# Performance work log

Measured on AMD Instinct MI355X. Metric: run time of the kernel, lower is better.

Reference implementation:

```python
import jax, jax.numpy as jnp
import numpy as np

F, G, S, E, P, B, T = 1024, 512, 512, 256, 8, 256, 256

def _gru(x, h, W_ih, W_hh, b_ih, b_hh):
    # torch.nn.GRUCell math; gate order r, z, n
    gi = x @ W_ih.T + b_ih
    gh = h @ W_hh.T + b_hh
    ir, iz, inn = jnp.split(gi, 3, axis=1)
    hr, hz, hn = jnp.split(gh, 3, axis=1)
    r = jax.nn.sigmoid(ir + hr)
    z = jax.nn.sigmoid(iz + hz)
    n = jnp.tanh(inn + r * hn)
    return (1.0 - z) * n + z * h

def setup_inputs() -> dict:
    key = jax.random.key(0)
    ks = jax.random.split(key, 16)
    feature_ = jax.random.normal(ks[0], (B, F), dtype=jnp.float32)
    spk_id = jax.random.randint(ks[1], (B,), 0, P)
    speaker_mask = jax.nn.one_hot(spk_id, P, dtype=jnp.float32)
    global_history = jax.random.normal(ks[2], (T, B, G), dtype=jnp.float32)
    speaker0 = jax.random.normal(ks[3], (B, P, S), dtype=jnp.float32)
    emotion0 = jax.random.normal(ks[4], (B, E), dtype=jnp.float32)
    sc = 0.05
    return {
        "feature_": feature_, "speaker_mask": speaker_mask,
        "global_history": global_history, "speaker0": speaker0, "emotion0": emotion0,
        "Wg_ih": jax.random.normal(ks[5], (3 * G, F + S)) * sc,
        "Wg_hh": jax.random.normal(ks[6], (3 * G, G)) * sc,
        "bg_ih": jnp.zeros((3 * G,)), "bg_hh": jnp.zeros((3 * G,)),
        "Wp_ih": jax.random.normal(ks[7], (3 * S, F + G)) * sc,
        "Wp_hh": jax.random.normal(ks[8], (3 * S, S)) * sc,
        "bp_ih": jnp.zeros((3 * S,)), "bp_hh": jnp.zeros((3 * S,)),
        "We_ih": jax.random.normal(ks[9], (3 * E, S)) * sc,
        "We_hh": jax.random.normal(ks[10], (3 * E, E)) * sc,
        "be_ih": jnp.zeros((3 * E,)), "be_hh": jnp.zeros((3 * E,)),
        "attn_W": jax.random.normal(ks[11], (G, F)) * sc,
    }

def reference(feature_, speaker_mask, global_history, speaker0, emotion0,
              Wg_ih, Wg_hh, bg_ih, bg_hh,
              Wp_ih, Wp_hh, bp_ih, bp_hh,
              We_ih, We_hh, be_ih, be_hh, attn_W):
    b = feature_.shape[0]
    p = speaker_mask.shape[1]
    spk_id = jnp.argmax(speaker_mask, axis=1)                      # (B,)
    rows = jnp.arange(b)
    sel0 = speaker0[rows, spk_id]                                   # select_parties -> (B, S)
    feature_speak = jnp.concatenate([feature_, sel0], axis=1)       # (B, F+S)
    global_state = _gru(feature_speak, global_history[-1], Wg_ih, Wg_hh, bg_ih, bg_hh)
    # attention over global history (T > 0 path); dropout = identity (eval)
    x_ = feature_ @ attn_W.T                                        # (B, G)
    alpha = jax.nn.softmax(jnp.einsum('bg,tbg->bt', x_, global_history), axis=1)
    context = jnp.einsum('bt,tbg->bg', alpha, global_history)       # (B, G)
    feature_context = jnp.concatenate([feature_, context], axis=1)  # (B, F+G)
    fc = jnp.broadcast_to(feature_context[:, None, :], (b, p, feature_context.shape[1]))
    fc = fc.reshape(b * p, -1)
    parties_state = _gru(fc, speaker0.reshape(b * p, -1), Wp_ih, Wp_hh, bp_ih, bp_hh)
    parties_state = parties_state.reshape(b, p, -1)                 # (B, P, S)
    m = speaker_mask[:, :, None]
    speaker = speaker0 * (1.0 - m) + parties_state * m
    parties = speaker[rows, spk_id]                                 # (B, S)
    emotion = _gru(parties, emotion0, We_ih, We_hh, be_ih, be_hh)
    return emotion, global_state, speaker
```

## Files before the change

### kernel.cpp

```cpp
#include <hip/hip_runtime.h>
#include <hip/hip_bf16.h>
#include <math.h>

#define BB 256
#define FF 1024
#define GG 512
#define SS 512
#define EE 256
#define PP 8
#define TT 256

typedef __attribute__((ext_vector_type(8))) short bs8;
typedef __attribute__((ext_vector_type(4))) float f32x4;

__device__ __forceinline__ float sigmoidf_(float x) { return 1.0f / (1.0f + expf(-x)); }

__device__ __forceinline__ short f2bf(float f) {
    union { float f; unsigned u; } v; v.f = f;
    unsigned r = v.u + 0x7FFFu + ((v.u >> 16) & 1u);
    return (short)(r >> 16);
}

union BPack { bs8 s; __hip_bfloat162 h[4]; };

__device__ __forceinline__ bs8 ld8cvt(const float* p) {
    float4 a = *(const float4*)p, b = *(const float4*)(p + 4);
    BPack u;
    u.h[0] = __float22bfloat162_rn({a.x, a.y});
    u.h[1] = __float22bfloat162_rn({a.z, a.w});
    u.h[2] = __float22bfloat162_rn({b.x, b.y});
    u.h[3] = __float22bfloat162_rn({b.z, b.w});
    return u.s;
}
__device__ __forceinline__ void ld8split(const float* p, bs8& ho, bs8& lo) {
    float4 a = *(const float4*)p, b = *(const float4*)(p + 4);
    float v[8] = {a.x, a.y, a.z, a.w, b.x, b.y, b.z, b.w};
    BPack uh, ul;
#pragma unroll
    for (int j = 0; j < 4; ++j) {
        __hip_bfloat162 h2 = __float22bfloat162_rn({v[2*j], v[2*j+1]});
        uh.h[j] = h2;
        float r0 = v[2*j]   - __low2float(h2);
        float r1 = v[2*j+1] - __high2float(h2);
        ul.h[j] = __float22bfloat162_rn({r0, r1});
    }
    ho = uh.s; lo = ul.s;
}

#define OWG_IH 0L
#define OWG_HH 2359296L
#define OWP_IH 3145728L
#define OWP_HH 5505024L
#define OWE_IH 6291456L
#define OWE_HH 6684672L
#define WTOT   6881280L

#define MB1 3360
#define MB2 3616
#define MB3 3744
#define MB4 3808
#define MB5 3840
#define MB6 4096
#define MBE 5120

__global__ __launch_bounds__(256) void k_mega(
        const float* __restrict__ Wg_ih, const float* __restrict__ Wg_hh,
        const float* __restrict__ Wp_ih, const float* __restrict__ Wp_hh,
        const float* __restrict__ We_ih, const float* __restrict__ We_hh,
        const float* __restrict__ attn_W, const float* __restrict__ feature_,
        const float* __restrict__ h_g, const float* __restrict__ emotion0,
        const float* __restrict__ mask, const float* __restrict__ sp0,
        short* __restrict__ Wbf, short* __restrict__ awhi, short* __restrict__ awlo,
        short* __restrict__ xg, short* __restrict__ fhi, short* __restrict__ flo,
        short* __restrict__ hg_bf, short* __restrict__ emo_bf, short* __restrict__ sel0_bf,
        float* __restrict__ sel0, int* __restrict__ spk, float* __restrict__ speaker_out) {
    int blk = blockIdx.x, tid = threadIdx.x;
    if (blk < MB1) {
        long i = (long)blk * 2048 + tid * 8;
        const float* src; long base;
        if      (i < OWG_HH) { src = Wg_ih; base = OWG_IH; }
        else if (i < OWP_IH) { src = Wg_hh; base = OWG_HH; }
        else if (i < OWP_HH) { src = Wp_ih; base = OWP_IH; }
        else if (i < OWE_IH) { src = Wp_hh; base = OWP_HH; }
        else if (i < OWE_HH) { src = We_ih; base = OWE_IH; }
        else                 { src = We_hh; base = OWE_HH; }
        *(bs8*)(Wbf + i) = ld8cvt(src + (i - base));
    } else if (blk < MB2) {
        long i = (long)(blk - MB1) * 2048 + tid * 8;
        bs8 h, l;
        ld8split(attn_W + i, h, l);
        *(bs8*)(awhi + i) = h;
        *(bs8*)(awlo + i) = l;
    } else if (blk < MB3) {
        long i = (long)(blk - MB2) * 2048 + tid * 8;
        bs8 h, l;
        ld8split(feature_ + i, h, l);
        *(bs8*)(fhi + i) = h;
        *(bs8*)(flo + i) = l;
        long b = i >> 10, c = i & 1023;
        *(bs8*)(xg + b * 1536 + c) = h;
    } else if (blk < MB4) {
        long i = (long)(blk - MB3) * 2048 + tid * 8;
        *(bs8*)(hg_bf + i) = ld8cvt(h_g + i);
    } else if (blk < MB5) {
        long i = (long)(blk - MB4) * 2048 + tid * 8;
        *(bs8*)(emo_bf + i) = ld8cvt(emotion0 + i);
    } else if (blk < MB6) {
        int b = blk - MB5;
        __shared__ int sid;
        if (tid == 0) {
            int best = 0; float bv = mask[b * PP];
            for (int p = 1; p < PP; ++p) { float v = mask[b * PP + p]; if (v > bv) { bv = v; best = p; } }
            sid = best; spk[b] = best;
        }
        __syncthreads();
        const float* src = sp0 + ((size_t)b * PP + sid) * SS;
        for (int j = tid; j < SS; j += 256) {
            float v = src[j];
            sel0[(size_t)b * SS + j] = v;
            short h = f2bf(v);
            sel0_bf[(size_t)b * SS + j] = h;
            xg[(size_t)b * 1536 + FF + j] = h;
        }
    } else {
        size_t i = ((size_t)(blk - MB6) * 256 + tid) * 4;
        *(float4*)(speaker_out + i) = *(const float4*)(sp0 + i);
    }
}

struct GDesc {
    const short *A, *A2, *W, *Wl;
    float* C;
    int lda, lda2, kb, ldw, woff, ldc, K, nbn, flags;
};
struct GBatch {
    GDesc d[6];
    int start[7];
    int ng;
};

__global__ __launch_bounds__(256) void k_bgemm(GBatch gb) {
    __shared__ __align__(16) short Ash[64 * 64], Bsh[64 * 64];
    __shared__ __align__(16) short Asl[64 * 64], Bsl[64 * 64];

    int bid = blockIdx.x;
    int g = 0;
    while (g + 1 < gb.ng && bid >= gb.start[g + 1]) ++g;
    GDesc d = gb.d[g];
    int local = bid - gb.start[g];
    int bn = local % d.nbn, bm = local / d.nbn;
    const bool split = (d.flags & 1) != 0;

    const int tid = threadIdx.x;
    const int lane = tid & 63, wid = tid >> 6;
    const int wr = wid >> 1, wc = wid & 1;
    const int r0 = tid >> 3, c0 = tid & 7;
    const int r1 = r0 + 32;
    const int la = lane & 15, lk = lane >> 4;
    const int sw = la & 7;

    f32x4 acc[2][2] = {};

    for (int k0 = 0; k0 < d.K; k0 += 64) {
        bs8 ah0, ah1, bh0, bh1, al0, al1, bl0, bl1;
        if (split) {
            size_t oa0 = (size_t)(bm * 64 + r0) * d.lda + k0 + c0 * 8;
            size_t oa1 = (size_t)(bm * 64 + r1) * d.lda + k0 + c0 * 8;
            size_t ow0 = (size_t)(bn * 64 + r0) * d.ldw + d.woff + k0 + c0 * 8;
            size_t ow1 = (size_t)(bn * 64 + r1) * d.ldw + d.woff + k0 + c0 * 8;
            ah0 = *(const bs8*)(d.A + oa0);  ah1 = *(const bs8*)(d.A + oa1);
            al0 = *(const bs8*)(d.A2 + oa0); al1 = *(const bs8*)(d.A2 + oa1);
            bh0 = *(const bs8*)(d.W + ow0);  bh1 = *(const bs8*)(d.W + ow1);
            bl0 = *(const bs8*)(d.Wl + ow0); bl1 = *(const bs8*)(d.Wl + ow1);
        } else {
            const short* Ab; int alda;
            if (k0 < d.kb) { Ab = d.A + k0; alda = d.lda; }
            else           { Ab = d.A2 + (k0 - d.kb); alda = d.lda2; }
            ah0 = *(const bs8*)(Ab + (size_t)(bm * 64 + r0) * alda + c0 * 8);
            ah1 = *(const bs8*)(Ab + (size_t)(bm * 64 + r1) * alda + c0 * 8);
            bh0 = *(const bs8*)(d.W + (size_t)(bn * 64 + r0) * d.ldw + d.woff + k0 + c0 * 8);
            bh1 = *(const bs8*)(d.W + (size_t)(bn * 64 + r1) * d.ldw + d.woff + k0 + c0 * 8);
        }
        __syncthreads();
        *(bs8*)(Ash + r0 * 64 + ((c0 ^ (r0 & 7)) * 8)) = ah0;
        *(bs8*)(Ash + r1 * 64 + ((c0 ^ (r1 & 7)) * 8)) = ah1;
        *(bs8*)(Bsh + r0 * 64 + ((c0 ^ (r0 & 7)) * 8)) = bh0;
        *(bs8*)(Bsh + r1 * 64 + ((c0 ^ (r1 & 7)) * 8)) = bh1;
        if (split) {
            *(bs8*)(Asl + r0 * 64 + ((c0 ^ (r0 & 7)) * 8)) = al0;
            *(bs8*)(Asl + r1 * 64 + ((c0 ^ (r1 & 7)) * 8)) = al1;
            *(bs8*)(Bsl + r0 * 64 + ((c0 ^ (r0 & 7)) * 8)) = bl0;
            *(bs8*)(Bsl + r1 * 64 + ((c0 ^ (r1 & 7)) * 8)) = bl1;
        }
        __syncthreads();
#pragma unroll
        for (int kk = 0; kk < 2; ++kk) {
            int slot = kk * 4 + lk;
            int off = (slot ^ sw) * 8;
            bs8 a0 = *(const bs8*)(Ash + (wr * 32 + la) * 64      + off);
            bs8 a1 = *(const bs8*)(Ash + (wr * 32 + 16 + la) * 64 + off);
            bs8 b0 = *(const bs8*)(Bsh + (wc * 32 + la) * 64      + off);
            bs8 b1 = *(const bs8*)(Bsh + (wc * 32 + 16 + la) * 64 + off);
            acc[0][0] = __builtin_amdgcn_mfma_f32_16x16x32_bf16(a0, b0, acc[0][0], 0, 0, 0);
            acc[0][1] = __builtin_amdgcn_mfma_f32_16x16x32_bf16(a0, b1, acc[0][1], 0, 0, 0);
            acc[1][0] = __builtin_amdgcn_mfma_f32_16x16x32_bf16(a1, b0, acc[1][0], 0, 0, 0);
            acc[1][1] = __builtin_amdgcn_mfma_f32_16x16x32_bf16(a1, b1, acc[1][1], 0, 0, 0);
            if (split) {
                bs8 xl0 = *(const bs8*)(Asl + (wr * 32 + la) * 64      + off);
                bs8 xl1 = *(const bs8*)(Asl + (wr * 32 + 16 + la) * 64 + off);
                bs8 yl0 = *(const bs8*)(Bsl + (wc * 32 + la) * 64      + off);
                bs8 yl1 = *(const bs8*)(Bsl + (wc * 32 + 16 + la) * 64 + off);
                acc[0][0] = __builtin_amdgcn_mfma_f32_16x16x32_bf16(a0, yl0, acc[0][0], 0, 0, 0);
                acc[0][0] = __builtin_amdgcn_mfma_f32_16x16x32_bf16(xl0, b0, acc[0][0], 0, 0, 0);
                acc[0][1] = __builtin_amdgcn_mfma_f32_16x16x32_bf16(a0, yl1, acc[0][1], 0, 0, 0);
                acc[0][1] = __builtin_amdgcn_mfma_f32_16x16x32_bf16(xl0, b1, acc[0][1], 0, 0, 0);
                acc[1][0] = __builtin_amdgcn_mfma_f32_16x16x32_bf16(a1, yl0, acc[1][0], 0, 0, 0);
                acc[1][0] = __builtin_amdgcn_mfma_f32_16x16x32_bf16(xl1, b0, acc[1][0], 0, 0, 0);
                acc[1][1] = __builtin_amdgcn_mfma_f32_16x16x32_bf16(a1, yl1, acc[1][1], 0, 0, 0);
                acc[1][1] = __builtin_amdgcn_mfma_f32_16x16x32_bf16(xl1, b1, acc[1][1], 0, 0, 0);
            }
        }
    }

    const int rowb = (lane >> 4) * 4, coln = lane & 15;
    const bool accum = (d.flags & 2) != 0;
#pragma unroll
    for (int i = 0; i < 2; ++i)
#pragma unroll
    for (int j = 0; j < 2; ++j)
#pragma unroll
    for (int r = 0; r < 4; ++r) {
        int row = bm * 64 + wr * 32 + i * 16 + rowb + r;
        int col = bn * 64 + wc * 32 + j * 16 + coln;
        size_t idx = (size_t)row * d.ldc + col;
        if (accum) d.C[idx] += acc[i][j][r];
        else       d.C[idx]  = acc[i][j][r];
    }
}

__global__ __launch_bounds__(256) void k_attnp(const float* __restrict__ x_,
                                               const float* __restrict__ gh,
                                               float* __restrict__ ctxp,
                                               float2* __restrict__ msb) {
    int blk = blockIdx.x;
    int b = blk & (BB - 1), ch = blk >> 8;
    int tid = threadIdx.x, w = tid >> 6, lane = tid & 63;
    __shared__ float wm[4], ws[4];
    __shared__ float part[4][GG];

    const float* xb = x_ + (size_t)b * GG + lane * 8;
    float4 xa = *(const float4*)xb;
    float4 xc = *(const float4*)(xb + 4);

    float m = -INFINITY, s = 0.f;
    float acc[8] = {};
    int t0 = ch * 32 + w * 8;
#pragma unroll
    for (int it = 0; it < 8; ++it) {
        int t = t0 + it;
        const float* row = gh + ((size_t)t * BB + b) * GG + lane * 8;
        float4 v1 = *(const float4*)row;
        float4 v2 = *(const float4*)(row + 4);
        float p = v1.x*xa.x + v1.y*xa.y + v1.z*xa.z + v1.w*xa.w
                + v2.x*xc.x + v2.y*xc.y + v2.z*xc.z + v2.w*xc.w;
#pragma unroll
        for (int off = 32; off; off >>= 1) p += __shfl_xor(p, off);
        float nm = fmaxf(m, p);
        float scale = expf(m - nm);
        float e = expf(p - nm);
        s = s * scale + e;
        acc[0] = acc[0]*scale + e*v1.x; acc[1] = acc[1]*scale + e*v1.y;
        acc[2] = acc[2]*scale + e*v1.z; acc[3] = acc[3]*scale + e*v1.w;
        acc[4] = acc[4]*scale + e*v2.x; acc[5] = acc[5]*scale + e*v2.y;
        acc[6] = acc[6]*scale + e*v2.z; acc[7] = acc[7]*scale + e*v2.w;
        m = nm;
    }
    if (lane == 0) { wm[w] = m; ws[w] = s; }
    *(float4*)&part[w][lane * 8]     = make_float4(acc[0], acc[1], acc[2], acc[3]);
    *(float4*)&part[w][lane * 8 + 4] = make_float4(acc[4], acc[5], acc[6], acc[7]);
    __syncthreads();

    float M = fmaxf(fmaxf(wm[0], wm[1]), fmaxf(wm[2], wm[3]));
    float f0 = expf(wm[0] - M), f1 = expf(wm[1] - M);
    float f2 = expf(wm[2] - M), f3 = expf(wm[3] - M);
    if (tid == 0) {
        float S = ws[0]*f0 + ws[1]*f1 + ws[2]*f2 + ws[3]*f3;
        msb[blk] = make_float2(M, S);
    }
    for (int j = tid; j < GG; j += 256) {
        float r = part[0][j]*f0 + part[1][j]*f1 + part[2][j]*f2 + part[3][j]*f3;
        ctxp[(size_t)blk * GG + j] = r;
    }
}

__global__ __launch_bounds__(256) void k_attnm(const float* __restrict__ ctxp,
                                               const float2* __restrict__ msb,
                                               short* __restrict__ ctx_bf) {
    int b = blockIdx.x, tid = threadIdx.x;
    float mv[8], sv[8];
    float M = -INFINITY;
#pragma unroll
    for (int c = 0; c < 8; ++c) {
        float2 t = msb[c * BB + b];
        mv[c] = t.x; sv[c] = t.y;
        M = fmaxf(M, t.x);
    }
    float S = 0.f;
    float f[8];
#pragma unroll
    for (int c = 0; c < 8; ++c) { f[c] = expf(mv[c] - M); S += sv[c] * f[c]; }
    float inv = 1.0f / S;
#pragma unroll
    for (int c = 0; c < 8; ++c) f[c] *= inv;
    for (int j = tid; j < GG; j += 256) {
        float r = 0.f;
#pragma unroll
        for (int c = 0; c < 8; ++c) r += ctxp[(size_t)(c * BB + b) * GG + j] * f[c];
        ctx_bf[(size_t)b * GG + j] = f2bf(r);
    }
}

__global__ __launch_bounds__(256) void k_gru2(
        const float* __restrict__ gi_g, const float* __restrict__ gh_g,
        const float* __restrict__ bg_ih, const float* __restrict__ bg_hh,
        const float* __restrict__ hg, float* __restrict__ global_out,
        const float* __restrict__ gi_p, const float* __restrict__ gh_p,
        const float* __restrict__ bp_ih, const float* __restrict__ bp_hh,
        const float* __restrict__ sel0, const int* __restrict__ spk,
        short* __restrict__ par_bf, float* __restrict__ speaker_out) {
    int idx = blockIdx.x * 256 + threadIdx.x;
    if (idx < BB * GG) {
        int b = idx / GG, j = idx - b * GG;
        const float* gib = gi_g + (size_t)b * 3 * GG;
        const float* ghb = gh_g + (size_t)b * 3 * GG;
        float r = sigmoidf_(gib[j] + bg_ih[j] + ghb[j] + bg_hh[j]);
        float z = sigmoidf_(gib[GG + j] + bg_ih[GG + j] + ghb[GG + j] + bg_hh[GG + j]);
        float n = tanhf(gib[2*GG + j] + bg_ih[2*GG + j] + r * (ghb[2*GG + j] + bg_hh[2*GG + j]));
        global_out[idx] = (1.0f - z) * n + z * hg[idx];
    } else {
        idx -= BB * GG;
        int b = idx / SS, j = idx - b * SS;
        const float* gib = gi_p + (size_t)b * 3 * SS;
        const float* ghb = gh_p + (size_t)b * 3 * SS;
        float r = sigmoidf_(gib[j] + bp_ih[j] + ghb[j] + bp_hh[j]);
        float z = sigmoidf_(gib[SS + j] + bp_ih[SS + j] + ghb[SS + j] + bp_hh[SS + j]);
        float n = tanhf(gib[2*SS + j] + bp_ih[2*SS + j] + r * (ghb[2*SS + j] + bp_hh[2*SS + j]));
        float o = (1.0f - z) * n + z * sel0[idx];
        par_bf[idx] = f2bf(o);
        speaker_out[((size_t)b * PP + spk[b]) * SS + j] = o;
    }
}

__global__ __launch_bounds__(256) void k_gru(const float* __restrict__ gi, const float* __restrict__ gh,
                                             const float* __restrict__ bih, const float* __restrict__ bhh,
                                             const float* __restrict__ h,
                                             float* __restrict__ out, int H) {
    int idx = blockIdx.x * 256 + threadIdx.x;
    int b = idx / H, j = idx - b * H;
    const float* gib = gi + (size_t)b * 3 * H;
    const float* ghb = gh + (size_t)b * 3 * H;
    float r = sigmoidf_(gib[j] + bih[j] + ghb[j] + bhh[j]);
    float z = sigmoidf_(gib[H + j] + bih[H + j] + ghb[H + j] + bhh[H + j]);
    float n = tanhf(gib[2 * H + j] + bih[2 * H + j] + r * (ghb[2 * H + j] + bhh[2 * H + j]));
    out[idx] = (1.0f - z) * n + z * h[idx];
}

extern "C" void kernel_launch(void* const* d_in, const int* in_sizes, int n_in,
                              void* d_out, int out_size, void* d_ws, size_t ws_size,
                              hipStream_t stream) {
    const float* feature_ = (const float*)d_in[0];
    const float* mask     = (const float*)d_in[1];
    const float* ghist    = (const float*)d_in[2];
    const float* speaker0 = (const float*)d_in[3];
    const float* emotion0 = (const float*)d_in[4];
    const float* Wg_ih    = (const float*)d_in[5];
    const float* Wg_hh    = (const float*)d_in[6];
    const float* bg_ih    = (const float*)d_in[7];
    const float* bg_hh    = (const float*)d_in[8];
    const float* Wp_ih    = (const float*)d_in[9];
    const float* Wp_hh    = (const float*)d_in[10];
    const float* bp_ih    = (const float*)d_in[11];
    const float* bp_hh    = (const float*)d_in[12];
    const float* We_ih    = (const float*)d_in[13];
    const float* We_hh    = (const float*)d_in[14];
    const float* be_ih    = (const float*)d_in[15];
    const float* be_hh    = (const float*)d_in[16];
    const float* attn_W   = (const float*)d_in[17];

    float* out = (float*)d_out;
    float* emotion_out = out;
    float* global_out  = out + (size_t)BB * EE;
    float* speaker_out = global_out + (size_t)BB * GG;

    char* cur = (char*)d_ws;
    short* Wbf     = (short*)cur; cur += (size_t)WTOT * 2;
    short* awhi    = (short*)cur; cur += (size_t)GG * FF * 2;
    short* awlo    = (short*)cur; cur += (size_t)GG * FF * 2;
    short* xg      = (short*)cur; cur += (size_t)BB * 1536 * 2;
    short* fhi     = (short*)cur; cur += (size_t)BB * FF * 2;
    short* flo     = (short*)cur; cur += (size_t)BB * FF * 2;
    short* hg_bf   = (short*)cur; cur += (size_t)BB * GG * 2;
    short* emo_bf  = (short*)cur; cur += (size_t)BB * EE * 2;
    short* sel0_bf = (short*)cur; cur += (size_t)BB * SS * 2;
    short* ctx_bf  = (short*)cur; cur += (size_t)BB * GG * 2;
    short* par_bf  = (short*)cur; cur += (size_t)BB * SS * 2;

    float* sel0    = (float*)cur; cur += (size_t)BB * SS * 4;
    float* x_      = (float*)cur; cur += (size_t)BB * GG * 4;
    float* ctxp    = (float*)cur; cur += (size_t)2048 * GG * 4;
    float2* msb    = (float2*)cur; cur += (size_t)2048 * 8;
    float* gi_g    = (float*)cur; cur += (size_t)BB * 3 * GG * 4;
    float* gh_g    = (float*)cur; cur += (size_t)BB * 3 * GG * 4;
    float* gi_p    = (float*)cur; cur += (size_t)BB * 3 * SS * 4;
    float* gh_p    = (float*)cur; cur += (size_t)BB * 3 * SS * 4;
    float* gi_e    = (float*)cur; cur += (size_t)BB * 3 * EE * 4;
    float* gh_e    = (float*)cur; cur += (size_t)BB * 3 * EE * 4;
    int*   spk     = (int*)cur;   cur += 256 * 4;

    const float* h_g = ghist + (size_t)(TT - 1) * BB * GG;

    short* Wg_ih_bf = Wbf + OWG_IH;
    short* Wg_hh_bf = Wbf + OWG_HH;
    short* Wp_ih_bf = Wbf + OWP_IH;
    short* Wp_hh_bf = Wbf + OWP_HH;
    short* We_ih_bf = Wbf + OWE_IH;
    short* We_hh_bf = Wbf + OWE_HH;

    k_mega<<<MBE, 256, 0, stream>>>(Wg_ih, Wg_hh, Wp_ih, Wp_hh, We_ih, We_hh,
                                    attn_W, feature_, h_g, emotion0, mask, speaker0,
                                    Wbf, awhi, awlo, xg, fhi, flo, hg_bf, emo_bf,
                                    sel0_bf, sel0, spk, speaker_out);

    GBatch gbA;
    gbA.d[0] = { fhi, flo, awhi, awlo, x_, FF, FF, FF, FF, 0, GG, FF, 8, 1 };
    gbA.d[1] = { xg, xg, Wg_ih_bf, nullptr, gi_g, 1536, 1536, 1536, 1536, 0, 3*GG, 1536, 24, 0 };
    gbA.d[2] = { hg_bf, hg_bf, Wg_hh_bf, nullptr, gh_g, GG, GG, GG, GG, 0, 3*GG, GG, 24, 0 };
    gbA.d[3] = { sel0_bf, sel0_bf, Wp_hh_bf, nullptr, gh_p, SS, SS, SS, SS, 0, 3*SS, SS, 24, 0 };
    gbA.d[4] = { emo_bf, emo_bf, We_hh_bf, nullptr, gh_e, EE, EE, EE, EE, 0, 3*EE, EE, 12, 0 };
    gbA.d[5] = { xg, xg, Wp_ih_bf, nullptr, gi_p, 1536, 1536, 1536, 1536, 0, 3*SS, FF, 24, 0 };
    gbA.start[0] = 0;   gbA.start[1] = 32;  gbA.start[2] = 128; gbA.start[3] = 224;
    gbA.start[4] = 320; gbA.start[5] = 368; gbA.start[6] = 464;
    gbA.ng = 6;
    k_bgemm<<<464, 256, 0, stream>>>(gbA);

    k_attnp<<<2048, 256, 0, stream>>>(x_, ghist, ctxp, msb);

    k_attnm<<<BB, 256, 0, stream>>>(ctxp, msb, ctx_bf);

    GBatch gbB;
    gbB.d[0] = { ctx_bf, ctx_bf, Wp_ih_bf, nullptr, gi_p, GG, GG, GG, 1536, FF, 3*SS, GG, 24, 2 };
    gbB.start[0] = 0; gbB.start[1] = 96; gbB.ng = 1;
    k_bgemm<<<96, 256, 0, stream>>>(gbB);

    k_gru2<<<(BB * GG + BB * SS) / 256, 256, 0, stream>>>(
        gi_g, gh_g, bg_ih, bg_hh, h_g, global_out,
        gi_p, gh_p, bp_ih, bp_hh, sel0, spk, par_bf, speaker_out);

    GBatch gbC;
    gbC.d[0] = { par_bf, par_bf, We_ih_bf, nullptr, gi_e, SS, SS, SS, SS, 0, 3*EE, SS, 12, 0 };
    gbC.start[0] = 0; gbC.start[1] = 48; gbC.ng = 1;
    k_bgemm<<<48, 256, 0, stream>>>(gbC);

    k_gru<<<(BB * EE) / 256, 256, 0, stream>>>(gi_e, gh_e, be_ih, be_hh, emotion0, emotion_out, EE);
}
```

Before: 100.7 us.

## Fuse attention merge, context GEMM and GRU epilogues into two tail kernels

Replaces the chain of attention-merge, context GEMM, party GRU, emotion-input GEMM and emotion GRU kernels with two fused kernels. k_tail1 combines the softmax partials into a bf16 context tile in LDS, multiplies it against the context slice of Wp_ih with MFMA, and applies the party GRU in the epilogue while the global GRU runs on spare blocks. k_tail2 performs the emotion input GEMM with the GRU epilogue and also copies the untouched speaker rows, skipping the selected ones. This removes four launches and several global round trips for ctx_bf, gi_e and the accumulate pass. The cost is fewer blocks in the GEMM phases (32 and 16), which may underuse the GPU.

New measurement: 114.3 us. +13.5%, slower.

```diff
diff --git a/kernel.cpp b/kernel.cpp
--- a/kernel.cpp
+++ b/kernel.cpp
@@ -60,8 +60,7 @@
 #define MB3 3744
 #define MB4 3808
 #define MB5 3840
-#define MB6 4096
-#define MBE 5120
+#define MBE 4096
 
 __global__ __launch_bounds__(256) void k_mega(
         const float* __restrict__ Wg_ih, const float* __restrict__ Wg_hh,
@@ -73,7 +72,7 @@
         short* __restrict__ Wbf, short* __restrict__ awhi, short* __restrict__ awlo,
         short* __restrict__ xg, short* __restrict__ fhi, short* __restrict__ flo,
         short* __restrict__ hg_bf, short* __restrict__ emo_bf, short* __restrict__ sel0_bf,
-        float* __restrict__ sel0, int* __restrict__ spk, float* __restrict__ speaker_out) {
+        float* __restrict__ sel0, int* __restrict__ spk) {
     int blk = blockIdx.x, tid = threadIdx.x;
     if (blk < MB1) {
         long i = (long)blk * 2048 + tid * 8;
@@ -105,7 +104,7 @@
     } else if (blk < MB5) {
         long i = (long)(blk - MB4) * 2048 + tid * 8;
         *(bs8*)(emo_bf + i) = ld8cvt(emotion0 + i);
-    } else if (blk < MB6) {
+    } else {
         int b = blk - MB5;
         __shared__ int sid;
         if (tid == 0) {
@@ -122,9 +121,6 @@
             sel0_bf[(size_t)b * SS + j] = h;
             xg[(size_t)b * 1536 + FF + j] = h;
         }
-    } else {
-        size_t i = ((size_t)(blk - MB6) * 256 + tid) * 4;
-        *(float4*)(speaker_out + i) = *(const float4*)(sp0 + i);
     }
 }
 
@@ -223,7 +219,6 @@
     }
 
     const int rowb = (lane >> 4) * 4, coln = lane & 15;
-    const bool accum = (d.flags & 2) != 0;
 #pragma unroll
     for (int i = 0; i < 2; ++i)
 #pragma unroll
@@ -232,9 +227,7 @@
     for (int r = 0; r < 4; ++r) {
         int row = bm * 64 + wr * 32 + i * 16 + rowb + r;
         int col = bn * 64 + wc * 32 + j * 16 + coln;
-        size_t idx = (size_t)row * d.ldc + col;
-        if (accum) d.C[idx] += acc[i][j][r];
-        else       d.C[idx]  = acc[i][j][r];
+        d.C[(size_t)row * d.ldc + col] = acc[i][j][r];
     }
 }
 
@@ -293,43 +286,20 @@
     }
 }
 
-__global__ __launch_bounds__(256) void k_attnm(const float* __restrict__ ctxp,
-                                               const float2* __restrict__ msb,
-                                               short* __restrict__ ctx_bf) {
-    int b = blockIdx.x, tid = threadIdx.x;
-    float mv[8], sv[8];
-    float M = -INFINITY;
-#pragma unroll
-    for (int c = 0; c < 8; ++c) {
-        float2 t = msb[c * BB + b];
-        mv[c] = t.x; sv[c] = t.y;
-        M = fmaxf(M, t.x);
-    }
-    float S = 0.f;
-    float f[8];
-#pragma unroll
-    for (int c = 0; c < 8; ++c) { f[c] = expf(mv[c] - M); S += sv[c] * f[c]; }
-    float inv = 1.0f / S;
-#pragma unroll
-    for (int c = 0; c < 8; ++c) f[c] *= inv;
-    for (int j = tid; j < GG; j += 256) {
-        float r = 0.f;
-#pragma unroll
-        for (int c = 0; c < 8; ++c) r += ctxp[(size_t)(c * BB + b) * GG + j] * f[c];
-        ctx_bf[(size_t)b * GG + j] = f2bf(r);
-    }
-}
-
-__global__ __launch_bounds__(256) void k_gru2(
-        const float* __restrict__ gi_g, const float* __restrict__ gh_g,
-        const float* __restrict__ bg_ih, const float* __restrict__ bg_hh,
-        const float* __restrict__ hg, float* __restrict__ global_out,
+#define T1G 32
+__global__ __launch_bounds__(256) void k_tail1(
+        const float* __restrict__ ctxp, const float2* __restrict__ msb,
+        const short* __restrict__ Wp_ih_bf,
         const float* __restrict__ gi_p, const float* __restrict__ gh_p,
         const float* __restrict__ bp_ih, const float* __restrict__ bp_hh,
         const float* __restrict__ sel0, const int* __restrict__ spk,
-        short* __restrict__ par_bf, float* __restrict__ speaker_out) {
-    int idx = blockIdx.x * 256 + threadIdx.x;
-    if (idx < BB * GG) {
+        short* __restrict__ par_bf, float* __restrict__ speaker_out,
+        const float* __restrict__ gi_g, const float* __restrict__ gh_g,
+        const float* __restrict__ bg_ih, const float* __restrict__ bg_hh,
+        const float* __restrict__ hg, float* __restrict__ global_out) {
+    int bid = blockIdx.x, tid = threadIdx.x;
+    if (bid >= T1G) {
+        int idx = (bid - T1G) * 256 + tid;
         int b = idx / GG, j = idx - b * GG;
         const float* gib = gi_g + (size_t)b * 3 * GG;
         const float* ghb = gh_g + (size_t)b * 3 * GG;
@@ -337,32 +307,206 @@
         float z = sigmoidf_(gib[GG + j] + bg_ih[GG + j] + ghb[GG + j] + bg_hh[GG + j]);
         float n = tanhf(gib[2*GG + j] + bg_ih[2*GG + j] + r * (ghb[2*GG + j] + bg_hh[2*GG + j]));
         global_out[idx] = (1.0f - z) * n + z * hg[idx];
-    } else {
-        idx -= BB * GG;
-        int b = idx / SS, j = idx - b * SS;
-        const float* gib = gi_p + (size_t)b * 3 * SS;
-        const float* ghb = gh_p + (size_t)b * 3 * SS;
-        float r = sigmoidf_(gib[j] + bp_ih[j] + ghb[j] + bp_hh[j]);
-        float z = sigmoidf_(gib[SS + j] + bp_ih[SS + j] + ghb[SS + j] + bp_hh[SS + j]);
-        float n = tanhf(gib[2*SS + j] + bp_ih[2*SS + j] + r * (ghb[2*SS + j] + bp_hh[2*SS + j]));
-        float o = (1.0f - z) * n + z * sel0[idx];
-        par_bf[idx] = f2bf(o);
-        speaker_out[((size_t)b * PP + spk[b]) * SS + j] = o;
-    }
-}
-
-__global__ __launch_bounds__(256) void k_gru(const float* __restrict__ gi, const float* __restrict__ gh,
-                                             const float* __restrict__ bih, const float* __restrict__ bhh,
-                                             const float* __restrict__ h,
-                                             float* __restrict__ out, int H) {
-    int idx = blockIdx.x * 256 + threadIdx.x;
-    int b = idx / H, j = idx - b * H;
-    const float* gib = gi + (size_t)b * 3 * H;
-    const float* ghb = gh + (size_t)b * 3 * H;
-    float r = sigmoidf_(gib[j] + bih[j] + ghb[j] + bhh[j]);
-    float z = sigmoidf_(gib[H + j] + bih[H + j] + ghb[H + j] + bhh[H + j]);
-    float n = tanhf(gib[2 * H + j] + bih[2 * H + j] + r * (ghb[2 * H + j] + bhh[2 * H + j]));
-    out[idx] = (1.0f - z) * n + z * h[idx];
+        return;
+    }
+
+    __shared__ __align__(16) short Actx[64 * 512];
+    __shared__ __align__(16) short Bs[3][64 * 64];
+    __shared__ float f_lds[64][8];
+
+    int bm = bid >> 3, bn = bid & 7;
+    int brow = bm * 64;
+
+    if (tid < 64) {
+        int b = brow + tid;
+        float mv[8], sv[8];
+        float M = -INFINITY;
+#pragma unroll
+        for (int c = 0; c < 8; ++c) {
+            float2 t = msb[c * BB + b];
+            mv[c] = t.x; sv[c] = t.y;
+            M = fmaxf(M, t.x);
+        }
+        float fv[8], S = 0.f;
+#pragma unroll
+        for (int c = 0; c < 8; ++c) { fv[c] = expf(mv[c] - M); S += sv[c] * fv[c]; }
+        float inv = 1.0f / S;
+#pragma unroll
+        for (int c = 0; c < 8; ++c) f_lds[tid][c] = fv[c] * inv;
+    }
+    __syncthreads();
+
+    for (int gidx = tid; gidx < 64 * 64; gidx += 256) {
+        int row = gidx >> 6, gr = gidx & 63;
+        int c64 = gr >> 3, slot = gr & 7;
+        int k = gr * 8;
+        int b = brow + row;
+        float a0 = 0.f, a1 = 0.f, a2 = 0.f, a3 = 0.f, a4 = 0.f, a5 = 0.f, a6 = 0.f, a7 = 0.f;
+#pragma unroll
+        for (int c = 0; c < 8; ++c) {
+            float fcb = f_lds[row][c];
+            const float* p = ctxp + ((size_t)(c * BB + b)) * GG + k;
+            float4 v1 = *(const float4*)p;
+            float4 v2 = *(const float4*)(p + 4);
+            a0 += fcb * v1.x; a1 += fcb * v1.y; a2 += fcb * v1.z; a3 += fcb * v1.w;
+            a4 += fcb * v2.x; a5 += fcb * v2.y; a6 += fcb * v2.z; a7 += fcb * v2.w;
+        }
+        BPack u;
+        u.h[0] = __float22bfloat162_rn({a0, a1});
+        u.h[1] = __float22bfloat162_rn({a2, a3});
+        u.h[2] = __float22bfloat162_rn({a4, a5});
+        u.h[3] = __float22bfloat162_rn({a6, a7});
+        *(bs8*)(Actx + row * 512 + c64 * 64 + ((slot ^ (row & 7)) * 8)) = u.s;
+    }
+    __syncthreads();
+
+    const int lane = tid & 63, wid = tid >> 6;
+    const int wr = wid >> 1, wc = wid & 1;
+    const int r0 = tid >> 3, c0 = tid & 7;
+    const int r1 = r0 + 32;
+    const int la = lane & 15, lk = lane >> 4;
+    const int sw = la & 7;
+
+    f32x4 acc[3][2][2] = {};
+
+    for (int k0 = 0; k0 < 512; k0 += 64) {
+        bs8 b0g[3], b1g[3];
+#pragma unroll
+        for (int g = 0; g < 3; ++g) {
+            b0g[g] = *(const bs8*)(Wp_ih_bf + (size_t)(g * 512 + bn * 64 + r0) * 1536 + FF + k0 + c0 * 8);
+            b1g[g] = *(const bs8*)(Wp_ih_bf + (size_t)(g * 512 + bn * 64 + r1) * 1536 + FF + k0 + c0 * 8);
+        }
+        __syncthreads();
+#pragma unroll
+        for (int g = 0; g < 3; ++g) {
+            *(bs8*)(Bs[g] + r0 * 64 + ((c0 ^ (r0 & 7)) * 8)) = b0g[g];
+            *(bs8*)(Bs[g] + r1 * 64 + ((c0 ^ (r1 & 7)) * 8)) = b1g[g];
+        }
+        __syncthreads();
+#pragma unroll
+        for (int kk = 0; kk < 2; ++kk) {
+            int slot = kk * 4 + lk;
+            int off = (slot ^ sw) * 8;
+            bs8 a0 = *(const bs8*)(Actx + (wr * 32 + la) * 512      + k0 + off);
+            bs8 a1 = *(const bs8*)(Actx + (wr * 32 + 16 + la) * 512 + k0 + off);
+#pragma unroll
+            for (int g = 0; g < 3; ++g) {
+                bs8 bb0 = *(const bs8*)(Bs[g] + (wc * 32 + la) * 64      + off);
+                bs8 bb1 = *(const bs8*)(Bs[g] + (wc * 32 + 16 + la) * 64 + off);
+                acc[g][0][0] = __builtin_amdgcn_mfma_f32_16x16x32_bf16(a0, bb0, acc[g][0][0], 0, 0, 0);
+                acc[g][0][1] = __builtin_amdgcn_mfma_f32_16x16x32_bf16(a0, bb1, acc[g][0][1], 0, 0, 0);
+                acc[g][1][0] = __builtin_amdgcn_mfma_f32_16x16x32_bf16(a1, bb0, acc[g][1][0], 0, 0, 0);
+                acc[g][1][1] = __builtin_amdgcn_mfma_f32_16x16x32_bf16(a1, bb1, acc[g][1][1], 0, 0, 0);
+            }
+        }
+    }
+
+    const int rowb = (lane >> 4) * 4, coln = lane & 15;
+#pragma unroll
+    for (int i = 0; i < 2; ++i)
+#pragma unroll
+    for (int r = 0; r < 4; ++r) {
+        int row = brow + wr * 32 + i * 16 + rowb + r;
+        int sp = spk[row];
+#pragma unroll
+        for (int j = 0; j < 2; ++j) {
+            int col = bn * 64 + wc * 32 + j * 16 + coln;
+            const float* gib = gi_p + (size_t)row * 1536;
+            const float* ghb = gh_p + (size_t)row * 1536;
+            float gr_ = sigmoidf_(acc[0][i][j][r] + gib[col] + bp_ih[col] + ghb[col] + bp_hh[col]);
+            float gz  = sigmoidf_(acc[1][i][j][r] + gib[512 + col] + bp_ih[512 + col] + ghb[512 + col] + bp_hh[512 + col]);
+            float gn  = tanhf(acc[2][i][j][r] + gib[1024 + col] + bp_ih[1024 + col] + gr_ * (ghb[1024 + col] + bp_hh[1024 + col]));
+            float o = (1.0f - gz) * gn + gz * sel0[(size_t)row * SS + col];
+            par_bf[(size_t)row * SS + col] = f2bf(o);
+            speaker_out[((size_t)row * PP + sp) * SS + col] = o;
+        }
+    }
+}
+
+#define T2G 16
+__global__ __launch_bounds__(256) void k_tail2(
+        const short* __restrict__ par_bf, const short* __restrict__ We_ih_bf,
+        const float* __restrict__ gh_e,
+        const float* __restrict__ be_ih, const float* __restrict__ be_hh,
+        const float* __restrict__ emotion0, float* __restrict__ emotion_out,
+        const float* __restrict__ sp0, const int* __restrict__ spk,
+        float* __restrict__ speaker_out) {
+    int bid = blockIdx.x, tid = threadIdx.x;
+    if (bid >= T2G) {
+        size_t i = ((size_t)(bid - T2G) * 256 + tid) * 4;
+        int b = (int)(i >> 12);
+        int p = (int)(i >> 9) & 7;
+        if (p != spk[b]) *(float4*)(speaker_out + i) = *(const float4*)(sp0 + i);
+        return;
+    }
+
+    __shared__ __align__(16) short Ash[64 * 64];
+    __shared__ __align__(16) short Bs[3][64 * 64];
+
+    int bm = bid >> 2, bn = bid & 3;
+    int brow = bm * 64;
+
+    const int lane = tid & 63, wid = tid >> 6;
+    const int wr = wid >> 1, wc = wid & 1;
+    const int r0 = tid >> 3, c0 = tid & 7;
+    const int r1 = r0 + 32;
+    const int la = lane & 15, lk = lane >> 4;
+    const int sw = la & 7;
+
+    f32x4 acc[3][2][2] = {};
+
+    for (int k0 = 0; k0 < 512; k0 += 64) {
+        bs8 ah0 = *(const bs8*)(par_bf + (size_t)(brow + r0) * 512 + k0 + c0 * 8);
+        bs8 ah1 = *(const bs8*)(par_bf + (size_t)(brow + r1) * 512 + k0 + c0 * 8);
+        bs8 b0g[3], b1g[3];
+#pragma unroll
+        for (int g = 0; g < 3; ++g) {
+            b0g[g] = *(const bs8*)(We_ih_bf + (size_t)(g * 256 + bn * 64 + r0) * 512 + k0 + c0 * 8);
+            b1g[g] = *(const bs8*)(We_ih_bf + (size_t)(g * 256 + bn * 64 + r1) * 512 + k0 + c0 * 8);
+        }
+        __syncthreads();
+        *(bs8*)(Ash + r0 * 64 + ((c0 ^ (r0 & 7)) * 8)) = ah0;
+        *(bs8*)(Ash + r1 * 64 + ((c0 ^ (r1 & 7)) * 8)) = ah1;
+#pragma unroll
+        for (int g = 0; g < 3; ++g) {
+            *(bs8*)(Bs[g] + r0 * 64 + ((c0 ^ (r0 & 7)) * 8)) = b0g[g];
+            *(bs8*)(Bs[g] + r1 * 64 + ((c0 ^ (r1 & 7)) * 8)) = b1g[g];
+        }
+        __syncthreads();
+#pragma unroll
+        for (int kk = 0; kk < 2; ++kk) {
+            int slot = kk * 4 + lk;
+            int off = (slot ^ sw) * 8;
+            bs8 a0 = *(const bs8*)(Ash + (wr * 32 + la) * 64      + off);
+            bs8 a1 = *(const bs8*)(Ash + (wr * 32 + 16 + la) * 64 + off);
+#pragma unroll
+            for (int g = 0; g < 3; ++g) {
+                bs8 bb0 = *(const bs8*)(Bs[g] + (wc * 32 + la) * 64      + off);
+                bs8 bb1 = *(const bs8*)(Bs[g] + (wc * 32 + 16 + la) * 64 + off);
+                acc[g][0][0] = __builtin_amdgcn_mfma_f32_16x16x32_bf16(a0, bb0, acc[g][0][0], 0, 0, 0);
+                acc[g][0][1] = __builtin_amdgcn_mfma_f32_16x16x32_bf16(a0, bb1, acc[g][0][1], 0, 0, 0);
+                acc[g][1][0] = __builtin_amdgcn_mfma_f32_16x16x32_bf16(a1, bb0, acc[g][1][0], 0, 0, 0);
+                acc[g][1][1] = __builtin_amdgcn_mfma_f32_16x16x32_bf16(a1, bb1, acc[g][1][1], 0, 0, 0);
+            }
+        }
+    }
+
+    const int rowb = (lane >> 4) * 4, coln = lane & 15;
+#pragma unroll
+    for (int i = 0; i < 2; ++i)
+#pragma unroll
+    for (int r = 0; r < 4; ++r) {
+        int row = brow + wr * 32 + i * 16 + rowb + r;
+#pragma unroll
+        for (int j = 0; j < 2; ++j) {
+            int col = bn * 64 + wc * 32 + j * 16 + coln;
+            const float* ghb = gh_e + (size_t)row * 768;
+            float gr_ = sigmoidf_(acc[0][i][j][r] + be_ih[col] + ghb[col] + be_hh[col]);
+            float gz  = sigmoidf_(acc[1][i][j][r] + be_ih[256 + col] + ghb[256 + col] + be_hh[256 + col]);
+            float gn  = tanhf(acc[2][i][j][r] + be_ih[512 + col] + gr_ * (ghb[512 + col] + be_hh[512 + col]));
+            emotion_out[(size_t)row * EE + col] = (1.0f - gz) * gn + gz * emotion0[(size_t)row * EE + col];
+        }
+    }
 }
 
 extern "C" void kernel_launch(void* const* d_in, const int* in_sizes, int n_in,
@@ -402,7 +546,6 @@
     short* hg_bf   = (short*)cur; cur += (size_t)BB * GG * 2;
     short* emo_bf  = (short*)cur; cur += (size_t)BB * EE * 2;
     short* sel0_bf = (short*)cur; cur += (size_t)BB * SS * 2;
-    short* ctx_bf  = (short*)cur; cur += (size_t)BB * GG * 2;
     short* par_bf  = (short*)cur; cur += (size_t)BB * SS * 2;
 
     float* sel0    = (float*)cur; cur += (size_t)BB * SS * 4;
@@ -413,7 +556,6 @@
     float* gh_g    = (float*)cur; cur += (size_t)BB * 3 * GG * 4;
     float* gi_p    = (float*)cur; cur += (size_t)BB * 3 * SS * 4;
     float* gh_p    = (float*)cur; cur += (size_t)BB * 3 * SS * 4;
-    float* gi_e    = (float*)cur; cur += (size_t)BB * 3 * EE * 4;
     float* gh_e    = (float*)cur; cur += (size_t)BB * 3 * EE * 4;
     int*   spk     = (int*)cur;   cur += 256 * 4;
 
@@ -429,7 +571,7 @@
     k_mega<<<MBE, 256, 0, stream>>>(Wg_ih, Wg_hh, Wp_ih, Wp_hh, We_ih, We_hh,
                                     attn_W, feature_, h_g, emotion0, mask, speaker0,
                                     Wbf, awhi, awlo, xg, fhi, flo, hg_bf, emo_bf,
-                                    sel0_bf, sel0, spk, speaker_out);
+                                    sel0_bf, sel0, spk);
 
     GBatch gbA;
     gbA.d[0] = { fhi, flo, awhi, awlo, x_, FF, FF, FF, FF, 0, GG, FF, 8, 1 };
@@ -445,21 +587,12 @@
 
     k_attnp<<<2048, 256, 0, stream>>>(x_, ghist, ctxp, msb);
 
-    k_attnm<<<BB, 256, 0, stream>>>(ctxp, msb, ctx_bf);
-
-    GBatch gbB;
-    gbB.d[0] = { ctx_bf, ctx_bf, Wp_ih_bf, nullptr, gi_p, GG, GG, GG, 1536, FF, 3*SS, GG, 24, 2 };
-    gbB.start[0] = 0; gbB.start[1] = 96; gbB.ng = 1;
-    k_bgemm<<<96, 256, 0, stream>>>(gbB);
-
-    k_gru2<<<(BB * GG + BB * SS) / 256, 256, 0, stream>>>(
-        gi_g, gh_g, bg_ih, bg_hh, h_g, global_out,
-        gi_p, gh_p, bp_ih, bp_hh, sel0, spk, par_bf, speaker_out);
-
-    GBatch gbC;
-    gbC.d[0] = { par_bf, par_bf, We_ih_bf, nullptr, gi_e, SS, SS, SS, SS, 0, 3*EE, SS, 12, 0 };
-    gbC.start[0] = 0; gbC.start[1] = 48; gbC.ng = 1;
-    k_bgemm<<<48, 256, 0, stream>>>(gbC);
-
-    k_gru<<<(BB * EE) / 256, 256, 0, stream>>>(gi_e, gh_e, be_ih, be_hh, emotion0, emotion_out, EE);
-}
+    k_tail1<<<T1G + (BB * GG) / 256, 256, 0, stream>>>(
+        ctxp, msb, Wp_ih_bf, gi_p, gh_p, bp_ih, bp_hh, sel0, spk,
+        par_bf, speaker_out,
+        gi_g, gh_g, bg_ih, bg_hh, h_g, global_out);
+
+    k_tail2<<<T2G + (BB * PP * SS) / 4 / 256, 256, 0, stream>>>(
+        par_bf, We_ih_bf, gh_e, be_ih, be_hh, emotion0, emotion_out,
+        speaker0, spk, speaker_out);
+}
```
